# Kernel optimization log

Measured on AMD Instinct MI355X. Metric: run time of the kernel, lower is better.

The kernel has to match this reference:

```python
import jax, jax.numpy as jnp
import numpy as np

EPS = 1e-5
ABIT = 8
WBIT = 8


def ste_round(x):
    # straight-through rounding (HAWQ SymmetricQuantFunction)
    return x + jax.lax.stop_gradient(jnp.round(x) - x)


def quant_act(x, bit=ABIT):
    # per-tensor symmetric activation quantization (QuantAct)
    n = 2.0 ** (bit - 1) - 1  # 127
    scale = jnp.max(jnp.abs(x)) / n
    x_int = jnp.clip(ste_round(x / scale), -n - 1, n)
    return x_int * scale, scale


def setup_inputs() -> dict:
    key = jax.random.key(0)
    k = jax.random.split(key, 6)
    B, C_in, H, W, C_out = 32, 512, 32, 32, 128
    x = jax.random.normal(k[0], (B, C_in, H, W), jnp.float32)
    # incoming activation scale (input assumed already 8-bit quantized)
    act_scaling_factor = (jnp.max(jnp.abs(x)) / 127.0).reshape(1)
    bn_gamma = jax.random.uniform(k[1], (C_in,), jnp.float32, 0.5, 1.5)
    bn_beta = jax.random.normal(k[2], (C_in,), jnp.float32) * 0.1
    bn_mean = jax.random.normal(k[3], (C_in,), jnp.float32) * 0.1
    bn_var = jax.random.uniform(k[4], (C_in,), jnp.float32, 0.5, 1.5)
    conv_weight = jax.random.normal(k[5], (C_out, C_in, 3, 3), jnp.float32) / np.sqrt(C_in * 9)
    return {"x": x, "act_scaling_factor": act_scaling_factor,
            "bn_gamma": bn_gamma, "bn_beta": bn_beta,
            "bn_mean": bn_mean, "bn_var": bn_var,
            "conv_weight": conv_weight}


def reference(x, act_scaling_factor, bn_gamma, bn_beta, bn_mean, bn_var, conv_weight):
    nw = 2.0 ** (WBIT - 1) - 1  # 127
    s_in = act_scaling_factor.reshape(())

    # ---- QuantBn: fold BN into per-channel affine, quantize weight/bias ----
    w_bn = bn_gamma / jnp.sqrt(bn_var + EPS)            # [C_in]
    b_bn = bn_beta - bn_mean * w_bn                      # [C_in]
    ws_bn = jnp.max(jnp.abs(w_bn)) / nw                  # per-tensor weight scale
    w_int = jnp.clip(ste_round(w_bn / ws_bn), -nw - 1, nw)
    bn_sf = ws_bn * s_in                                 # bn output scaling factor
    b_int = ste_round(b_bn / bn_sf)
    x_int = x / s_in
    x = (x_int * w_int[None, :, None, None] + b_int[None, :, None, None]) * bn_sf

    # ---- ReLU ----
    x = jax.nn.relu(x)

    # ---- QuantAct: requantize activations to 8 bit ----
    x, s_act = quant_act(x)

    # ---- QuantConv2d: per-output-channel 8-bit weight quant, int conv ----
    ws_c = jnp.max(jnp.abs(conv_weight), axis=(1, 2, 3)) / nw       # [C_out]
    w_cint = jnp.clip(ste_round(conv_weight / ws_c[:, None, None, None]), -nw - 1, nw)
    y_int = jax.lax.conv_general_dilated(
        x / s_act, w_cint, window_strides=(1, 1), padding=((1, 1), (1, 1)),
        dimension_numbers=("NCHW", "OIHW", "NCHW"))
    conv_sf = s_act * ws_c                               # [C_out]
    y = y_int * conv_sf[None, :, None, None]

    # ---- QuantAct output requant ----
    y, s_out = quant_act(y)
    return (y, s_out)
```

## Files before the change

kernel.cpp:

```cpp
#include <hip/hip_runtime.h>


typedef int v4i __attribute__((ext_vector_type(4)));

#define WS_A1    64
#define WS_B1    2112
#define WS_WSC   4160
#define WS_XMX   4672
#define WS_XMN   6720
#define WS_WQ    8768
#define WS_X2    598592
#define WS_ZROW  18424384

__device__ __forceinline__ float wave_max(float m) {
#pragma unroll
    for (int off = 32; off; off >>= 1) m = fmaxf(m, __shfl_xor(m, off));
    return m;
}

__device__ __forceinline__ void stage16(const char* g, char* s, int lane) {
#if defined(__has_builtin) && __has_builtin(__builtin_amdgcn_global_load_lds)
    __builtin_amdgcn_global_load_lds(
        (const __attribute__((address_space(1))) void*)g,
        (__attribute__((address_space(3))) void*)s, 16, 0, 0);
#else
    *(v4i*)(s + lane * 16) = *(const v4i*)g;
#endif
}

__global__ __launch_bounds__(512) void k_prep(
    const float* __restrict__ gamma, const float* __restrict__ beta,
    const float* __restrict__ mean,  const float* __restrict__ var,
    const float* __restrict__ asf,   const float* __restrict__ cw,
    const float4* __restrict__ x4,
    float* ws_f, unsigned* ws_u, float* __restrict__ wsc,
    signed char* __restrict__ wq) {
    int t = threadIdx.x;
    int bid = blockIdx.x;
    __shared__ float red[16];
    if (bid < 512) {
        int c = bid;
        float mx = -3.4e38f, mn = 3.4e38f;
#pragma unroll
        for (int r = 0; r < 16; ++r) {
            int bbb = r * 2 + (t >> 8);
            float4 v = x4[((size_t)(bbb * 512 + c)) * 256 + (t & 255)];
            mx = fmaxf(mx, fmaxf(fmaxf(v.x, v.y), fmaxf(v.z, v.w)));
            mn = fminf(mn, fminf(fminf(v.x, v.y), fminf(v.z, v.w)));
        }
        mx = wave_max(mx);
        mn = -wave_max(-mn);
        if ((t & 63) == 0) { red[t >> 6] = mx; red[8 + (t >> 6)] = mn; }
        __syncthreads();
        if (t == 0) {
            float M = red[0], N = red[8];
#pragma unroll
            for (int i = 1; i < 8; ++i) { M = fmaxf(M, red[i]); N = fminf(N, red[8 + i]); }
            ws_f[WS_XMX / 4 + c] = M;
            ws_f[WS_XMN / 4 + c] = N;
        }
    } else if (bid < 640) {
        int co = bid - 512;
        const float* w = cw + (size_t)co * 4608;
        float m = 0.f;
        for (int j = t; j < 4608; j += 512) m = fmaxf(m, fabsf(w[j]));
        m = wave_max(m);
        if ((t & 63) == 0) red[t >> 6] = m;
        __syncthreads();
        float mall = red[0];
#pragma unroll
        for (int i = 1; i < 8; ++i) mall = fmaxf(mall, red[i]);
        float sc = mall / 127.0f;
        if (t == 0) wsc[co] = sc;
        int ci = t >> 6, cq = (t >> 4) & 3, cb = t & 15;
#pragma unroll
        for (int tap = 0; tap < 9; ++tap) {
            float q = fminf(fmaxf(rintf(w[t * 9 + tap] / sc), -128.f), 127.f);
            wq[(((size_t)(tap * 8 + ci) * 4 + cq) * 128 + co) * 16 + cb] = (signed char)q;
        }
    } else {
        float wbn = gamma[t] / sqrtf(var[t] + 1e-5f);
        float bbn = beta[t] - mean[t] * wbn;
        float m = wave_max(fabsf(wbn));
        if ((t & 63) == 0) red[t >> 6] = m;
        __syncthreads();
        float mall = red[0];
#pragma unroll
        for (int i = 1; i < 8; ++i) mall = fmaxf(mall, red[i]);
        float ws_bn = mall / 127.0f;
        float s_in  = asf[0];
        float bn_sf = ws_bn * s_in;
        float wint  = fminf(fmaxf(rintf(wbn / ws_bn), -128.f), 127.f);
        float bint  = rintf(bbn / bn_sf);
        ws_f[WS_A1 / 4 + t] = wint * bn_sf / s_in;
        ws_f[WS_B1 / 4 + t] = bint * bn_sf;
        if (t == 0) ws_u[1] = 0u;
    }
}

__global__ __launch_bounds__(256) void k_xquant(
    const float4* __restrict__ x4, float* __restrict__ ws_f,
    unsigned* __restrict__ x2u, unsigned* __restrict__ zrowu) {
    int bb = 31 - (blockIdx.x >> 5), h = blockIdx.x & 31;
    const float* A1 = ws_f + WS_A1 / 4;
    const float* B1 = ws_f + WS_B1 / 4;
    const float* XMX = ws_f + WS_XMX / 4;
    const float* XMN = ws_f + WS_XMN / 4;
    int t = threadIdx.x;

    __shared__ float sred[4];
    float cand = 0.f;
#pragma unroll
    for (int c0 = 0; c0 < 512; c0 += 256) {
        int c = c0 + t;
        float A = A1[c], B = B1[c];
        cand = fmaxf(cand, fmaxf(fmaf(XMX[c], A, B), fmaf(XMN[c], A, B)));
    }
    cand = wave_max(cand);
    if ((t & 63) == 0) sred[t >> 6] = cand;
    __syncthreads();
    float xm = fmaxf(fmaxf(sred[0], sred[1]), fmaxf(sred[2], sred[3]));
    float inv_sact = 127.0f / xm;
    if (blockIdx.x == 0 && t == 0) ws_f[3] = xm / 127.0f;

    size_t rowd = (size_t)(bb * 32 + h) * 4352;
    {
        int p = t >> 3, side = (t >> 2) & 1, d = t & 3;
        x2u[rowd + (p * 34 + side * 33) * 4 + d] = 0u;
    }
    if (blockIdx.x < 17) {
        int idx = blockIdx.x * 256 + t;
        if (idx < 4352) zrowu[idx] = 0u;
    }

    __shared__ unsigned lds[512 * 9];

#pragma unroll
    for (int it = 0; it < 16; ++it) {
        int idx = it * 256 + t;
        int c = idx >> 3, f4 = idx & 7;
        float4 v = x4[((size_t)bb * 512 + c) * 256 + h * 8 + f4];
        float A = A1[c] * inv_sact, B = B1[c] * inv_sact;
        unsigned q0 = (unsigned)(int)fminf(rintf(fmaxf(fmaf(v.x, A, B), 0.f)), 127.f);
        unsigned q1 = (unsigned)(int)fminf(rintf(fmaxf(fmaf(v.y, A, B), 0.f)), 127.f);
        unsigned q2 = (unsigned)(int)fminf(rintf(fmaxf(fmaf(v.z, A, B), 0.f)), 127.f);
        unsigned q3 = (unsigned)(int)fminf(rintf(fmaxf(fmaf(v.w, A, B), 0.f)), 127.f);
        lds[c * 9 + f4] = q0 | (q1 << 8) | (q2 << 16) | (q3 << 24);
    }
    __syncthreads();

#pragma unroll
    for (int it = 0; it < 4; ++it) {
        int p = it * 8 + (t >> 5);
        int s = (t >> 2) & 7;
        int k = t & 3;
        unsigned L[16];
#pragma unroll
        for (int j = 0; j < 16; ++j) L[j] = lds[(p * 16 + j) * 9 + s];
        uint4 o;
        unsigned* op = (unsigned*)&o;
#pragma unroll
        for (int d = 0; d < 4; ++d)
            op[d] = ((L[4 * d] >> (8 * k)) & 255u) |
                    (((L[4 * d + 1] >> (8 * k)) & 255u) << 8) |
                    (((L[4 * d + 2] >> (8 * k)) & 255u) << 16) |
                    (((L[4 * d + 3] >> (8 * k)) & 255u) << 24);
        *(uint4*)(x2u + rowd + (size_t)(p * 34 + s * 4 + 1 + k) * 4) = o;
    }
}

__global__ __launch_bounds__(256, 4) void k_conv(
    const unsigned char* __restrict__ x2, const unsigned char* __restrict__ zrow,
    const signed char* __restrict__ wq,
    const float* __restrict__ wsc, const float* __restrict__ ws_f,
    unsigned* __restrict__ amaxy, float* __restrict__ y) {
    __shared__ char ldsb[36864];
    int t = threadIdx.x;
    int lane = t & 63, wv = t >> 6;
    int nh = wv & 1, wr = wv >> 1;
    int m = lane & 15, quad = lane >> 4;

    int bid = blockIdx.x;
    int tile = (bid & 7) * 128 + (bid >> 3);
    int ch = tile & 1;
    int rg = (tile >> 1) & 15;
    int bb = tile >> 5;
    int co0 = ch * 64;
    int h0 = rg * 2;

    const unsigned char* xb = x2 + (size_t)bb * (32 * 17408);
    const v4i* rpt[4];
#pragma unroll
    for (int j = 0; j < 4; ++j) {
        int row = h0 - 1 + j;
        rpt[j] = (const v4i*)(((unsigned)row < 32u) ? (xb + (size_t)row * 17408) : zrow);
    }

    v4i acc[2][2];
#pragma unroll
    for (int i = 0; i < 2; ++i)
#pragma unroll
        for (int j = 0; j < 2; ++j) acc[i][j] = (v4i){0, 0, 0, 0};

    int abase = quad * 34 + m;
    const v4i* bv = (const v4i*)ldsb;

    for (int ci = 0; ci < 8; ++ci) {
        __syncthreads();
#pragma unroll
        for (int i = 0; i < 9; ++i) {
            int c = wv * 9 + i;
            int tap = c >> 2, cq = c & 3;
            const char* g = (const char*)wq +
                ((((size_t)(tap * 8 + ci) * 4 + cq) * 128 + co0) * 16) + lane * 16;
            stage16(g, ldsb + (c << 10), lane);
        }
        __syncthreads();

#pragma unroll
        for (int kh = 0; kh < 3; ++kh)
#pragma unroll
            for (int kw = 0; kw < 3; ++kw) {
                int tap = kh * 3 + kw;
                v4i a0 = rpt[wr + kh][ci * 136 + abase + kw];
                v4i a1 = rpt[wr + kh][ci * 136 + abase + kw + 16];
#pragma unroll
                for (int nt = 0; nt < 2; ++nt) {
                    v4i bf = bv[(tap * 4 + quad) * 64 + nh * 32 + nt * 16 + m];
                    acc[0][nt] = __builtin_amdgcn_mfma_i32_16x16x64_i8(a0, bf, acc[0][nt], 0, 0, 0);
                    acc[1][nt] = __builtin_amdgcn_mfma_i32_16x16x64_i8(a1, bf, acc[1][nt], 0, 0, 0);
                }
            }
    }

    float s_act = ws_f[3];
    float mx = 0.f;
    int row = h0 + wr;
#pragma unroll
    for (int nt = 0; nt < 2; ++nt) {
        int co = co0 + nh * 32 + nt * 16 + m;
        float sf = s_act * wsc[co];
        float* yb = y + ((size_t)(bb * 128 + co)) * 1024 + row * 32;
#pragma unroll
        for (int mt = 0; mt < 2; ++mt) {
            float4 vv;
            vv.x = (float)acc[mt][nt][0] * sf;
            vv.y = (float)acc[mt][nt][1] * sf;
            vv.z = (float)acc[mt][nt][2] * sf;
            vv.w = (float)acc[mt][nt][3] * sf;
            *(float4*)(yb + mt * 16 + quad * 4) = vv;
            mx = fmaxf(mx, fmaxf(fmaxf(fabsf(vv.x), fabsf(vv.y)),
                                 fmaxf(fabsf(vv.z), fabsf(vv.w))));
        }
    }
    mx = wave_max(mx);
    __syncthreads();
    if (lane == 0) ((float*)ldsb)[wv] = mx;
    __syncthreads();
    if (t == 0) {
        float* r = (float*)ldsb;
        float M = fmaxf(fmaxf(r[0], r[1]), fmaxf(r[2], r[3]));
        atomicMax(amaxy, __float_as_uint(M));
    }
}

__global__ __launch_bounds__(256) void k_yquant(float* __restrict__ yout,
                                                const unsigned* __restrict__ ws_u) {
    float s_out = __uint_as_float(ws_u[1]) / 127.0f;
    float4* y4 = (float4*)yout;
    int stride = gridDim.x * blockDim.x;
    for (int i = blockIdx.x * blockDim.x + threadIdx.x; i < 1048576; i += stride) {
        float4 v = y4[i];
        v.x = fminf(fmaxf(rintf(v.x / s_out), -128.f), 127.f) * s_out;
        v.y = fminf(fmaxf(rintf(v.y / s_out), -128.f), 127.f) * s_out;
        v.z = fminf(fmaxf(rintf(v.z / s_out), -128.f), 127.f) * s_out;
        v.w = fminf(fmaxf(rintf(v.w / s_out), -128.f), 127.f) * s_out;
        y4[i] = v;
    }
    if (blockIdx.x == 0 && threadIdx.x == 0) yout[4194304] = s_out;
}

extern "C" void kernel_launch(void* const* d_in, const int* in_sizes, int n_in,
                              void* d_out, int out_size, void* d_ws, size_t ws_size,
                              hipStream_t stream) {
    const float* x     = (const float*)d_in[0];
    const float* asf   = (const float*)d_in[1];
    const float* gamma = (const float*)d_in[2];
    const float* beta  = (const float*)d_in[3];
    const float* mean  = (const float*)d_in[4];
    const float* var   = (const float*)d_in[5];
    const float* cw    = (const float*)d_in[6];

    float*    ws_f = (float*)d_ws;
    unsigned* ws_u = (unsigned*)d_ws;
    signed char*   wq   = (signed char*)d_ws + WS_WQ;
    unsigned char* x2   = (unsigned char*)d_ws + WS_X2;
    unsigned char* zrow = (unsigned char*)d_ws + WS_ZROW;
    float* y = (float*)d_out;

    k_prep<<<641, 512, 0, stream>>>(gamma, beta, mean, var, asf, cw,
                                    (const float4*)x, ws_f, ws_u,
                                    ws_f + WS_WSC / 4, wq);
    k_xquant<<<1024, 256, 0, stream>>>((const float4*)x, ws_f,
                                       (unsigned*)x2, (unsigned*)zrow);
    k_conv<<<1024, 256, 0, stream>>>(x2, zrow, wq, ws_f + WS_WSC / 4,
                                     ws_f, ws_u + 1, y);
    k_yquant<<<1024, 256, 0, stream>>>(y, ws_u);
}
```

Measured before the change: 167.2 us.

## Double-buffer conv weight staging and enlarge per-block tile to four rows

The conv kernel now double-buffers the weight slices in LDS, prefetching the next input-channel chunk while MFMAs run on the current one, and drops one barrier per iteration. Each block also covers four output rows instead of two, with each wave computing all 64 output channels for half a row pair, so every B fragment loaded from LDS is reused across more MFMAs. The grid is halved to 512 blocks and LDS doubled to 72KB, which lowers occupancy (launch bounds go from 4 to 2 blocks per CU) and raises register pressure from the doubled accumulators.

```diff
diff --git a/kernel.cpp b/kernel.cpp
--- a/kernel.cpp
+++ b/kernel.cpp
@@ -169,24 +169,24 @@
     }
 }
 
-__global__ __launch_bounds__(256, 4) void k_conv(
+__global__ __launch_bounds__(256, 2) void k_conv(
     const unsigned char* __restrict__ x2, const unsigned char* __restrict__ zrow,
     const signed char* __restrict__ wq,
     const float* __restrict__ wsc, const float* __restrict__ ws_f,
     unsigned* __restrict__ amaxy, float* __restrict__ y) {
-    __shared__ char ldsb[36864];
+    __shared__ char ldsb[73728];
     int t = threadIdx.x;
     int lane = t & 63, wv = t >> 6;
-    int nh = wv & 1, wr = wv >> 1;
+    int wh = wv & 1, rp = wv >> 1;
     int m = lane & 15, quad = lane >> 4;
 
     int bid = blockIdx.x;
-    int tile = (bid & 7) * 128 + (bid >> 3);
+    int tile = (bid & 7) * 64 + (bid >> 3);
     int ch = tile & 1;
-    int rg = (tile >> 1) & 15;
-    int bb = tile >> 5;
+    int rg = (tile >> 1) & 7;
+    int bb = tile >> 4;
     int co0 = ch * 64;
-    int h0 = rg * 2;
+    int h0 = rg * 4 + rp * 2;
 
     const unsigned char* xb = x2 + (size_t)bb * (32 * 17408);
     const v4i* rpt[4];
@@ -196,65 +196,75 @@
         rpt[j] = (const v4i*)(((unsigned)row < 32u) ? (xb + (size_t)row * 17408) : zrow);
     }
 
-    v4i acc[2][2];
+    v4i acc[2][4];
 #pragma unroll
     for (int i = 0; i < 2; ++i)
 #pragma unroll
-        for (int j = 0; j < 2; ++j) acc[i][j] = (v4i){0, 0, 0, 0};
-
-    int abase = quad * 34 + m;
-    const v4i* bv = (const v4i*)ldsb;
-
+        for (int j = 0; j < 4; ++j) acc[i][j] = (v4i){0, 0, 0, 0};
+
+    int abase = quad * 34 + m + wh * 16;
+
+#pragma unroll
+    for (int i = 0; i < 9; ++i) {
+        int c = wv * 9 + i;
+        int tap = c >> 2, cq = c & 3;
+        const char* g = (const char*)wq +
+            ((((size_t)(tap * 8 + 0) * 4 + cq) * 128 + co0) * 16) + lane * 16;
+        stage16(g, ldsb + (c << 10), lane);
+    }
+    __syncthreads();
+
+#pragma unroll
     for (int ci = 0; ci < 8; ++ci) {
-        __syncthreads();
-#pragma unroll
-        for (int i = 0; i < 9; ++i) {
-            int c = wv * 9 + i;
-            int tap = c >> 2, cq = c & 3;
-            const char* g = (const char*)wq +
-                ((((size_t)(tap * 8 + ci) * 4 + cq) * 128 + co0) * 16) + lane * 16;
-            stage16(g, ldsb + (c << 10), lane);
-        }
-        __syncthreads();
-
+        if (ci < 7) {
+#pragma unroll
+            for (int i = 0; i < 9; ++i) {
+                int c = wv * 9 + i;
+                int tap = c >> 2, cq = c & 3;
+                const char* g = (const char*)wq +
+                    ((((size_t)(tap * 8 + ci + 1) * 4 + cq) * 128 + co0) * 16) + lane * 16;
+                stage16(g, ldsb + ((ci + 1) & 1) * 36864 + (c << 10), lane);
+            }
+        }
+        const v4i* bv = (const v4i*)(ldsb + (ci & 1) * 36864);
 #pragma unroll
         for (int kh = 0; kh < 3; ++kh)
 #pragma unroll
             for (int kw = 0; kw < 3; ++kw) {
                 int tap = kh * 3 + kw;
-                v4i a0 = rpt[wr + kh][ci * 136 + abase + kw];
-                v4i a1 = rpt[wr + kh][ci * 136 + abase + kw + 16];
-#pragma unroll
-                for (int nt = 0; nt < 2; ++nt) {
-                    v4i bf = bv[(tap * 4 + quad) * 64 + nh * 32 + nt * 16 + m];
+                v4i a0 = rpt[kh][ci * 136 + abase + kw];
+                v4i a1 = rpt[kh + 1][ci * 136 + abase + kw];
+#pragma unroll
+                for (int nt = 0; nt < 4; ++nt) {
+                    v4i bf = bv[(tap * 4 + quad) * 64 + nt * 16 + m];
                     acc[0][nt] = __builtin_amdgcn_mfma_i32_16x16x64_i8(a0, bf, acc[0][nt], 0, 0, 0);
                     acc[1][nt] = __builtin_amdgcn_mfma_i32_16x16x64_i8(a1, bf, acc[1][nt], 0, 0, 0);
                 }
             }
+        __syncthreads();
     }
 
     float s_act = ws_f[3];
     float mx = 0.f;
-    int row = h0 + wr;
-#pragma unroll
-    for (int nt = 0; nt < 2; ++nt) {
-        int co = co0 + nh * 32 + nt * 16 + m;
+#pragma unroll
+    for (int nt = 0; nt < 4; ++nt) {
+        int co = co0 + nt * 16 + m;
         float sf = s_act * wsc[co];
-        float* yb = y + ((size_t)(bb * 128 + co)) * 1024 + row * 32;
-#pragma unroll
-        for (int mt = 0; mt < 2; ++mt) {
+#pragma unroll
+        for (int r = 0; r < 2; ++r) {
+            int row = h0 + r;
+            float* yb = y + ((size_t)(bb * 128 + co)) * 1024 + row * 32 + wh * 16;
             float4 vv;
-            vv.x = (float)acc[mt][nt][0] * sf;
-            vv.y = (float)acc[mt][nt][1] * sf;
-            vv.z = (float)acc[mt][nt][2] * sf;
-            vv.w = (float)acc[mt][nt][3] * sf;
-            *(float4*)(yb + mt * 16 + quad * 4) = vv;
+            vv.x = (float)acc[r][nt][0] * sf;
+            vv.y = (float)acc[r][nt][1] * sf;
+            vv.z = (float)acc[r][nt][2] * sf;
+            vv.w = (float)acc[r][nt][3] * sf;
+            *(float4*)(yb + quad * 4) = vv;
             mx = fmaxf(mx, fmaxf(fmaxf(fabsf(vv.x), fabsf(vv.y)),
                                  fmaxf(fabsf(vv.z), fabsf(vv.w))));
         }
     }
     mx = wave_max(mx);
-    __syncthreads();
     if (lane == 0) ((float*)ldsb)[wv] = mx;
     __syncthreads();
     if (t == 0) {
@@ -303,7 +313,7 @@
                                     ws_f + WS_WSC / 4, wq);
     k_xquant<<<1024, 256, 0, stream>>>((const float4*)x, ws_f,
                                        (unsigned*)x2, (unsigned*)zrow);
-    k_conv<<<1024, 256, 0, stream>>>(x2, zrow, wq, ws_f + WS_WSC / 4,
-                                     ws_f, ws_u + 1, y);
+    k_conv<<<512, 256, 0, stream>>>(x2, zrow, wq, ws_f + WS_WSC / 4,
+                                    ws_f, ws_u + 1, y);
     k_yquant<<<1024, 256, 0, stream>>>(y, ws_u);
 }
```

Result: faster. 159.2 us (-4.8%).
